# Kernel optimization log

Measured on AMD Instinct MI355X. Metric: run time of the kernel, lower is better.

Reference implementation:

```python
import jax, jax.numpy as jnp
import numpy as np

B, N, C, K = 8, 4096, 128, 16
EPS = 1e-5  # BatchNorm1d default eps


def setup_inputs() -> dict:
    key = jax.random.key(0)
    k0, k1, k2 = jax.random.split(key, 3)
    xyz = jax.random.normal(k0, (B, N, 3), jnp.float32)
    x = jax.random.normal(k1, (B, C, N), jnp.float32)
    # Conv1d(channel, channel, kernel_size=1, bias=False) weight -> [C_out, C_in]
    W = jax.random.normal(k2, (C, C), jnp.float32) / np.sqrt(C)
    gamma = jnp.ones((C,), jnp.float32)
    beta = jnp.zeros((C,), jnp.float32)
    running_mean = jnp.zeros((C,), jnp.float32)
    running_var = jnp.ones((C,), jnp.float32)
    return {"xyz": xyz, "x": x, "W": W, "gamma": gamma, "beta": beta,
            "running_mean": running_mean, "running_var": running_var}


def _knn_idx(xyz, k):
    # squared pairwise distances d2[b,i,j] = ||xyz[b,i]-xyz[b,j]||^2
    s = jnp.sum(xyz * xyz, axis=-1)                      # [B,N]
    d2 = s[:, :, None] + s[:, None, :] - 2.0 * jnp.einsum('bnd,bmd->bnm', xyz, xyz)
    # keops argKmin over dim=1; d2 is symmetric so top_k over the last axis is equivalent
    _, idx = jax.lax.top_k(-d2, k)                       # [B,N,K]
    return idx


def reference(xyz, x, W, gamma, beta, running_mean, running_var):
    idx = _knn_idx(xyz, K)                               # [B,N,K] int32
    x_t = jnp.transpose(x, (0, 2, 1))                    # [B,N,C]
    grouped = jax.vmap(lambda pts, i: pts[i])(x_t, idx)  # [B,N,K,C] gather
    g = jnp.transpose(grouped, (0, 3, 2, 1))             # [B,C,K,N]
    # 1x1 Conv1d (no bias): GEMM over channel dim
    y = jnp.einsum('oc,bckn->bokn', W, g)                # [B,C,K,N]
    # BatchNorm1d (inference form with running stats)
    scale = gamma * jax.lax.rsqrt(running_var + EPS)     # [C]
    y = y * scale[None, :, None, None] + (beta - running_mean * scale)[None, :, None, None]
    y = jax.nn.relu(y)
    return jnp.max(y, axis=2)                            # max over k neighbors -> [B,C,N]
```

## Files before the change

### kernel.cpp

```cpp
#include <hip/hip_runtime.h>
#include <hip/hip_bf16.h>

#define BATCH 8
#define NPTS  4096
#define CCH   128
#define KNN_K 16

typedef __attribute__((ext_vector_type(8))) short  bf16x8;
typedef __attribute__((ext_vector_type(4))) float  f32x4;


static __device__ __forceinline__ short f2bf(float v) {
    __hip_bfloat16 h = __float2bfloat16(v);
    return __builtin_bit_cast(short, h);
}

__global__ __launch_bounds__(256) void transpose_kernel(
    const float* __restrict__ x, short* __restrict__ xTb)
{
    __shared__ short tile[64 * 66];
    const int tid = threadIdx.x;
    const int b   = blockIdx.x >> 7;
    const int rem = blockIdx.x & 127;
    const int nt  = rem >> 1;
    const int ct  = rem & 1;

    #pragma unroll
    for (int it = 0; it < 16; ++it) {
        const int idx = it * 256 + tid;
        const int cc  = idx >> 6;
        const int nn  = idx & 63;
        const float v = x[(size_t)(b * CCH + ct * 64 + cc) * NPTS + nt * 64 + nn];
        tile[cc * 66 + nn] = f2bf(v);
    }
    __syncthreads();
    #pragma unroll
    for (int it = 0; it < 16; ++it) {
        const int idx = it * 256 + tid;
        const int nn  = idx >> 6;
        const int cc  = idx & 63;
        xTb[(size_t)(b * NPTS + nt * 64 + nn) * CCH + ct * 64 + cc] = tile[cc * 66 + nn];
    }
}

__global__ __launch_bounds__(256) void small_prep_kernel(
    const float* __restrict__ xyz, const float* __restrict__ W,
    const float* __restrict__ gamma, const float* __restrict__ beta,
    const float* __restrict__ rmean, const float* __restrict__ rvar,
    short* __restrict__ Wb, float* __restrict__ scale, float* __restrict__ bias,
    float4* __restrict__ pts)
{
    const int t = blockIdx.x * 256 + threadIdx.x;
    if (t < CCH * CCH) Wb[t] = f2bf(W[t]);
    if (t < CCH) {
        const float s = gamma[t] / sqrtf(rvar[t] + 1e-5f);
        scale[t] = s;
        bias[t]  = beta[t] - rmean[t] * s;
    }
    {
        #pragma clang fp contract(off)
        const float px = xyz[3 * t + 0];
        const float py = xyz[3 * t + 1];
        const float pz = xyz[3 * t + 2];
        const float s  = px * px + py * py + pz * pz;
        pts[t] = make_float4(px, py, pz, s);
    }
}

__global__ __launch_bounds__(256) void knn_kernel(
    const float4* __restrict__ pts, unsigned short* __restrict__ knn)
{
    const int lane = threadIdx.x & 63;
    const int wid  = threadIdx.x >> 6;
    const int g    = lane >> 4;
    const int s    = lane & 15;
    const int wq   = blockIdx.x * 16 + wid * 4;
    const int b    = wq >> 12;
    const int i    = (wq & 4095) + g;
    const float4* pb = pts + (b << 12);

    const float4 q = pb[i];

    float bd = 3.4e38f;
    int   bj = 0;
    float tau = 3.4e38f;
    const bool sgt0 = (s > 0);
    const int  gsh  = g << 4;

    auto process = [&](const float4& p0, const float4& p1,
                       const float4& p2, const float4& p3, const int jbase) {
        float dd[4];
        {
            #pragma clang fp contract(off)
            dd[0] = (q.w + p0.w) - 2.0f * (q.x * p0.x + q.y * p0.y + q.z * p0.z);
            dd[1] = (q.w + p1.w) - 2.0f * (q.x * p1.x + q.y * p1.y + q.z * p1.z);
            dd[2] = (q.w + p2.w) - 2.0f * (q.x * p2.x + q.y * p2.y + q.z * p2.z);
            dd[3] = (q.w + p3.w) - 2.0f * (q.x * p3.x + q.y * p3.y + q.z * p3.z);
        }
        #pragma unroll
        for (int c = 0; c < 4; ++c) {
            const unsigned long long mask = __ballot(dd[c] < tau);
            unsigned sub = (unsigned)((mask >> gsh) & 0xFFFFull);
            while (__any(sub != 0)) {
                const bool has = (sub != 0);
                const int  l   = has ? (__ffs(sub) - 1) : 0;
                const float dvr = __shfl(dd[c], l, 16);
                const float dv  = has ? dvr : 3.4e38f;
                const int   jv  = jbase + c * 16 + l;
                sub = has ? (sub & (sub - 1)) : 0u;
                const float pd = __shfl_up(bd, 1, 16);
                const int   pj = __shfl_up(bj, 1, 16);
                const bool lt  = dv < bd;
                const bool ltp = sgt0 && (dv < pd);
                bd = lt ? (ltp ? pd : dv) : bd;
                bj = lt ? (ltp ? pj : jv) : bj;
            }
        }
        tau = __shfl(bd, 15, 16);
    };

    const float4* lp = pb + s;
    float4 a0 = lp[0], a1 = lp[16], a2 = lp[32], a3 = lp[48];
    lp += 64;

    #pragma unroll 2
    for (int it = 0; it < 64; ++it) {
        const float4* np = (it < 63) ? lp : pb;
        const float4 n0 = np[0], n1 = np[16], n2 = np[32], n3 = np[48];
        process(a0, a1, a2, a3, it * 64);
        a0 = n0; a1 = n1; a2 = n2; a3 = n3;
        lp += 64;
    }

    unsigned short* o = knn + ((((size_t)b << 12) + i) << 4);
    o[s] = (unsigned short)bj;
}

__global__ __launch_bounds__(256) void zgemm_kernel(
    const short* __restrict__ xTb, const short* __restrict__ Wb,
    short* __restrict__ Zb)
{
    __shared__ short sW[CCH * 136];
    const int lane = threadIdx.x & 63;
    const int wid  = threadIdx.x >> 6;
    const int kl   = lane & 15;
    const int q8   = (lane >> 4) * 8;

    #pragma unroll
    for (int it = 0; it < 8; ++it) {
        const int e = (it * 256 + threadIdx.x) * 8;
        const int r = e >> 7, c = e & 127;
        *(bf16x8*)(sW + r * 136 + c) = *(const bf16x8*)(Wb + e);
    }

    const int    G    = blockIdx.x * 64 + wid * 16 + kl;
    const size_t arow = (size_t)G * CCH;
    __syncthreads();

    const f32x4 zero = {0.f, 0.f, 0.f, 0.f};
    f32x4 acc[8];
    #pragma unroll
    for (int t = 0; t < 8; ++t) acc[t] = zero;

    #pragma unroll
    for (int kk = 0; kk < 4; ++kk) {
        const bf16x8 a = *(const bf16x8*)(xTb + arow + kk * 32 + q8);
        #pragma unroll
        for (int t = 0; t < 8; ++t) {
            const bf16x8 bf = *(const bf16x8*)(sW + (t * 16 + kl) * 136 + kk * 32 + q8);
            acc[t] = __builtin_amdgcn_mfma_f32_16x16x32_bf16(a, bf, acc[t], 0, 0, 0);
        }
    }

    const int rbase = blockIdx.x * 64 + wid * 16 + (lane >> 4) * 4;
    #pragma unroll
    for (int t = 0; t < 8; ++t)
        #pragma unroll
        for (int r = 0; r < 4; ++r)
            Zb[(size_t)(rbase + r) * CCH + t * 16 + kl] = f2bf(acc[t][r]);
}

__global__ __launch_bounds__(256) void gmax_kernel(
    const short* __restrict__ Zb, const unsigned short* __restrict__ knn,
    const float* __restrict__ scale, const float* __restrict__ bias,
    float* __restrict__ out)
{
    __shared__ float sm[16][132];
    const int lane = threadIdx.x & 63;
    const int wid  = threadIdx.x >> 6;
    const int n0   = blockIdx.x * 16;
    const int b    = blockIdx.x >> 8;
    const float s0 = scale[2 * lane],   s1 = scale[2 * lane + 1];
    const float t0 = bias[2 * lane],    t1 = bias[2 * lane + 1];

    for (int p = 0; p < 4; ++p) {
        const int n = n0 + wid * 4 + p;
        const unsigned short* kr = knn + (size_t)n * 16;
        float m0 = 0.f, m1 = 0.f;
        #pragma unroll
        for (int k = 0; k < 16; ++k) {
            const int r = (int)kr[k];
            const unsigned v = *(const unsigned*)(Zb + ((size_t)(b * NPTS + r)) * CCH + 2 * lane);
            const float z0 = __uint_as_float(v << 16);
            const float z1 = __uint_as_float(v & 0xFFFF0000u);
            m0 = fmaxf(m0, s0 * z0 + t0);
            m1 = fmaxf(m1, s1 * z1 + t1);
        }
        sm[wid * 4 + p][2 * lane]     = m0;
        sm[wid * 4 + p][2 * lane + 1] = m1;
    }
    __syncthreads();

    const int c    = threadIdx.x & 127;
    const int half = threadIdx.x >> 7;
    float v[8];
    #pragma unroll
    for (int i = 0; i < 8; ++i) v[i] = sm[half * 8 + i][c];
    float4 f0 = {v[0], v[1], v[2], v[3]};
    float4 f1 = {v[4], v[5], v[6], v[7]};
    float* op = out + ((size_t)(b * CCH + c)) * NPTS + (n0 & 4095) + half * 8;
    *(float4*)op       = f0;
    *(float4*)(op + 4) = f1;
}

extern "C" void kernel_launch(void* const* d_in, const int* in_sizes, int n_in,
                              void* d_out, int out_size, void* d_ws, size_t ws_size,
                              hipStream_t stream)
{
    const float* xyz   = (const float*)d_in[0];
    const float* x     = (const float*)d_in[1];
    const float* W     = (const float*)d_in[2];
    const float* gamma = (const float*)d_in[3];
    const float* beta  = (const float*)d_in[4];
    const float* rmean = (const float*)d_in[5];
    const float* rvar  = (const float*)d_in[6];
    float* out = (float*)d_out;

    char* ws = (char*)d_ws;
    short*          xTb   = (short*)(ws);
    short*          Wb    = (short*)(ws + 8388608);
    float*          scale = (float*)(ws + 8421376);
    float*          bias  = (float*)(ws + 8421888);
    float4*         pts   = (float4*)(ws + 8422400);
    unsigned short* knn   = (unsigned short*)(ws + 8946688);
    short*          Zb    = (short*)(ws + 9995264);

    transpose_kernel<<<BATCH * 64 * 2, 256, 0, stream>>>(x, xTb);
    small_prep_kernel<<<BATCH * NPTS / 256, 256, 0, stream>>>(
        xyz, W, gamma, beta, rmean, rvar, Wb, scale, bias, pts);
    knn_kernel<<<BATCH * NPTS / 16, 256, 0, stream>>>(pts, knn);
    zgemm_kernel<<<BATCH * NPTS / 64, 256, 0, stream>>>(xTb, Wb, Zb);
    gmax_kernel<<<BATCH * NPTS / 16, 256, 0, stream>>>(Zb, knn, scale, bias, out);
}
```

Before: 132.1 us.

## Replace serial KNN insertion with buffered candidates and bitonic merge

The KNN kernel no longer inserts each surviving candidate one at a time through a shift-based sorted list. Survivors are compacted into a 16-slot per-group buffer with ds_permute. When the buffer would overflow, it is sorted with a bitonic network over packed (distance, index) keys using ds_swizzle and merged into the running top-16 list. This is meant to cut the serialized per-candidate loop and its divergence, at the cost of full sort-and-merge work on every flush and extra permute traffic.

```diff
diff --git a/kernel.cpp b/kernel.cpp
--- a/kernel.cpp
+++ b/kernel.cpp
@@ -66,6 +66,8 @@
         pts[t] = make_float4(px, py, pz, s);
     }
 }
+
+#define PK_(h, l) ((((unsigned long long)(h)) << 32) | (unsigned long long)(l))
 
 __global__ __launch_bounds__(256) void knn_kernel(
     const float4* __restrict__ pts, unsigned short* __restrict__ knn)
@@ -81,59 +83,101 @@
 
     const float4 q = pb[i];
 
-    float bd = 3.4e38f;
-    int   bj = 0;
-    float tau = 3.4e38f;
-    const bool sgt0 = (s > 0);
-    const int  gsh  = g << 4;
-
-    auto process = [&](const float4& p0, const float4& p1,
-                       const float4& p2, const float4& p3, const int jbase) {
-        float dd[4];
+    const unsigned SENT_HI = 0xFF7FFFFFu;
+    const unsigned SENT_LO = 0xFFFFFFFFu;
+
+    unsigned lhi = SENT_HI, llo = SENT_LO;
+    float bufD = 0.f;
+    int   bufJ = 0;
+    int   cnt  = 0;
+    float tau  = 3.4e38f;
+    const int gsh = g << 4;
+
+    auto flush = [&]() {
+        const unsigned u = __float_as_uint(bufD);
+        unsigned khi = (u & 0x80000000u) ? ~u : (u | 0x80000000u);
+        unsigned klo = (unsigned)bufJ;
+        const bool inval = (s >= cnt);
+        khi = inval ? SENT_HI : khi;
+        klo = inval ? SENT_LO : klo;
+        #define CE_(K, J, OFF) { \
+            const unsigned ohi = (unsigned)__builtin_amdgcn_ds_swizzle((int)khi, OFF); \
+            const unsigned olo = (unsigned)__builtin_amdgcn_ds_swizzle((int)klo, OFF); \
+            const bool olt = PK_(ohi, olo) < PK_(khi, klo); \
+            const bool sel = (((s & (J)) == 0) == ((s & (K)) == 0)); \
+            const bool tk  = sel ? olt : !olt; \
+            khi = tk ? ohi : khi; klo = tk ? olo : klo; }
+        CE_(2, 1, 0x041F)
+        CE_(4, 2, 0x081F)  CE_(4, 1, 0x041F)
+        CE_(8, 4, 0x101F)  CE_(8, 2, 0x081F)  CE_(8, 1, 0x041F)
+        CE_(16, 8, 0x201F) CE_(16, 4, 0x101F) CE_(16, 2, 0x081F) CE_(16, 1, 0x041F)
+        #undef CE_
         {
-            #pragma clang fp contract(off)
-            dd[0] = (q.w + p0.w) - 2.0f * (q.x * p0.x + q.y * p0.y + q.z * p0.z);
-            dd[1] = (q.w + p1.w) - 2.0f * (q.x * p1.x + q.y * p1.y + q.z * p1.z);
-            dd[2] = (q.w + p2.w) - 2.0f * (q.x * p2.x + q.y * p2.y + q.z * p2.z);
-            dd[3] = (q.w + p3.w) - 2.0f * (q.x * p3.x + q.y * p3.y + q.z * p3.z);
-        }
-        #pragma unroll
-        for (int c = 0; c < 4; ++c) {
-            const unsigned long long mask = __ballot(dd[c] < tau);
-            unsigned sub = (unsigned)((mask >> gsh) & 0xFFFFull);
-            while (__any(sub != 0)) {
-                const bool has = (sub != 0);
-                const int  l   = has ? (__ffs(sub) - 1) : 0;
-                const float dvr = __shfl(dd[c], l, 16);
-                const float dv  = has ? dvr : 3.4e38f;
-                const int   jv  = jbase + c * 16 + l;
-                sub = has ? (sub & (sub - 1)) : 0u;
-                const float pd = __shfl_up(bd, 1, 16);
-                const int   pj = __shfl_up(bj, 1, 16);
-                const bool lt  = dv < bd;
-                const bool ltp = sgt0 && (dv < pd);
-                bd = lt ? (ltp ? pd : dv) : bd;
-                bj = lt ? (ltp ? pj : jv) : bj;
-            }
-        }
-        tau = __shfl(bd, 15, 16);
+            const unsigned rhi = (unsigned)__builtin_amdgcn_ds_swizzle((int)khi, 0x3C1F);
+            const unsigned rlo = (unsigned)__builtin_amdgcn_ds_swizzle((int)klo, 0x3C1F);
+            const bool rlt = PK_(rhi, rlo) < PK_(lhi, llo);
+            lhi = rlt ? rhi : lhi; llo = rlt ? rlo : llo;
+        }
+        #define MC_(J, OFF) { \
+            const unsigned ohi = (unsigned)__builtin_amdgcn_ds_swizzle((int)lhi, OFF); \
+            const unsigned olo = (unsigned)__builtin_amdgcn_ds_swizzle((int)llo, OFF); \
+            const bool olt = PK_(ohi, olo) < PK_(lhi, llo); \
+            const bool tk  = ((s & (J)) == 0) ? olt : !olt; \
+            lhi = tk ? ohi : lhi; llo = tk ? olo : llo; }
+        MC_(8, 0x201F) MC_(4, 0x101F) MC_(2, 0x081F) MC_(1, 0x041F)
+        #undef MC_
+        const unsigned thi = (unsigned)__builtin_amdgcn_ds_swizzle((int)lhi, 0x01F0);
+        tau = __uint_as_float((thi & 0x80000000u) ? (thi & 0x7FFFFFFFu) : ~thi);
+        cnt = 0;
     };
+
+    #define SUB_(DD, C, JB) { \
+        const unsigned long long mask = __ballot((DD) < tau); \
+        if (mask) { \
+            const unsigned sub = (unsigned)((mask >> gsh) & 0xFFFFull); \
+            const int m = __popc(sub); \
+            if (__any(cnt + m > 15)) flush(); \
+            const bool surv = (sub >> s) & 1u; \
+            const int rank  = __popc(sub & ((1u << s) - 1u)); \
+            const int dest  = surv ? (cnt + rank) : 15;    \
+            const int addr  = (gsh | dest) << 2; \
+            const int nd = __builtin_amdgcn_ds_permute(addr, __float_as_int(DD)); \
+            const int nj = __builtin_amdgcn_ds_permute(addr, (JB) + ((C) << 4) + s); \
+            const bool got = (s >= cnt) & (s < cnt + m); \
+            bufD = got ? __int_as_float(nd) : bufD; \
+            bufJ = got ? nj : bufJ; \
+            cnt += m; \
+        } }
 
     const float4* lp = pb + s;
     float4 a0 = lp[0], a1 = lp[16], a2 = lp[32], a3 = lp[48];
     lp += 64;
 
-    #pragma unroll 2
+    #pragma unroll 1
     for (int it = 0; it < 64; ++it) {
         const float4* np = (it < 63) ? lp : pb;
         const float4 n0 = np[0], n1 = np[16], n2 = np[32], n3 = np[48];
-        process(a0, a1, a2, a3, it * 64);
+        float dd0, dd1, dd2, dd3;
+        {
+            #pragma clang fp contract(off)
+            dd0 = (q.w + a0.w) - 2.0f * (q.x * a0.x + q.y * a0.y + q.z * a0.z);
+            dd1 = (q.w + a1.w) - 2.0f * (q.x * a1.x + q.y * a1.y + q.z * a1.z);
+            dd2 = (q.w + a2.w) - 2.0f * (q.x * a2.x + q.y * a2.y + q.z * a2.z);
+            dd3 = (q.w + a3.w) - 2.0f * (q.x * a3.x + q.y * a3.y + q.z * a3.z);
+        }
+        const int jbase = it * 64;
+        SUB_(dd0, 0, jbase)
+        SUB_(dd1, 1, jbase)
+        SUB_(dd2, 2, jbase)
+        SUB_(dd3, 3, jbase)
         a0 = n0; a1 = n1; a2 = n2; a3 = n3;
         lp += 64;
     }
+    #undef SUB_
+    flush();
 
     unsigned short* o = knn + ((((size_t)b << 12) + i) << 4);
-    o[s] = (unsigned short)bj;
+    o[s] = (unsigned short)llo;
 }
 
 __global__ __launch_bounds__(256) void zgemm_kernel(
```

Measured after the change: 116.7 us. -11.6%, faster.
